# Optimization experiments

Measured on AMD Instinct MI355X. Metric: run time of the kernel, lower is better.

The kernel has to match this reference:

```python
import jax, jax.numpy as jnp
import numpy as np

B, H, W, D = 4, 64, 64, 384
M, P = 12, 9
DH = D // M             # 32 head dim
DFF = 3 * D             # 1152 FFN hidden
N = H * W               # 4096 queries (single level)


def setup_inputs():
    key = jax.random.key(0)
    ks = jax.random.split(key, 12)
    g = lambda k, s, sc=0.02: jax.random.normal(k, s, jnp.float32) * sc
    return {
        "x": jax.random.normal(ks[0], (B, D, H, W), jnp.float32),
        "qry_masks": jnp.zeros((B, H, W), jnp.float32),
        "so_w": g(ks[1], (M * P * 2, D)), "so_b": g(ks[2], (M * P * 2,)),
        "aw_w": g(ks[3], (M * P, D)), "aw_b": g(ks[4], (M * P,)),
        "vp_w": g(ks[5], (D, D)), "vp_b": jnp.zeros((D,), jnp.float32),
        "op_w": g(ks[6], (D, D)), "op_b": jnp.zeros((D,), jnp.float32),
        "ln1_g": jnp.ones((D,), jnp.float32), "ln1_b": jnp.zeros((D,), jnp.float32),
        "w1": g(ks[7], (DFF, D)), "w2": g(ks[8], (D, DFF)),
        "ln2_g": jnp.ones((D,), jnp.float32), "ln2_b": jnp.zeros((D,), jnp.float32),
        "level_embed": g(ks[9], (1, D), 1.0),
    }


def _layernorm(x, g, b, eps=1e-5):
    mu = x.mean(-1, keepdims=True)
    v = ((x - mu) ** 2).mean(-1, keepdims=True)
    return (x - mu) * jax.lax.rsqrt(v + eps) * g + b


def _sine_pos(mask):
    # mask: [B,H,W] bool. mmdet SinePositionalEncoding(num_feats=D//2, normalize=True)
    not_mask = (~mask).astype(jnp.float32)
    y = jnp.cumsum(not_mask, 1)
    x = jnp.cumsum(not_mask, 2)
    eps, scale = 1e-6, 2.0 * np.pi
    y = y / (y[:, -1:, :] + eps) * scale
    x = x / (x[:, :, -1:] + eps) * scale
    nf = D // 2
    dim_t = 10000.0 ** (2.0 * (jnp.arange(nf) // 2).astype(jnp.float32) / nf)
    px, py = x[..., None] / dim_t, y[..., None] / dim_t

    def interleave(p):
        return jnp.stack([jnp.sin(p[..., 0::2]), jnp.cos(p[..., 1::2])], -1).reshape(p.shape[:-1] + (nf,))

    return jnp.concatenate([interleave(py), interleave(px)], -1)  # [B,H,W,D]


def _bilinear_gather(v, px, py):
    # v: [B,M,HW,DH]; px,py: [B,M,NP] pixel coords (grid_sample align_corners=False, zero pad)
    x0 = jnp.floor(px); y0 = jnp.floor(py)
    lx, ly = px - x0, py - y0
    x0i, y0i = x0.astype(jnp.int32), y0.astype(jnp.int32)
    out = jnp.zeros(v.shape[:2] + (px.shape[-1], v.shape[-1]), v.dtype)
    for dx, dy, wgt in ((0, 0, (1 - lx) * (1 - ly)), (1, 0, lx * (1 - ly)),
                        (0, 1, (1 - lx) * ly), (1, 1, lx * ly)):
        xi, yi = x0i + dx, y0i + dy
        valid = ((xi >= 0) & (xi < W) & (yi >= 0) & (yi < H)).astype(v.dtype)
        idx = jnp.clip(yi, 0, H - 1) * W + jnp.clip(xi, 0, W - 1)
        g = jnp.take_along_axis(v, idx[..., None], axis=2)  # [B,M,NP,DH]
        out = out + (wgt * valid)[..., None] * g
    return out


def _msdeform_attn(q, value_in, ref, mask_flat,
                   so_w, so_b, aw_w, aw_b, vp_w, vp_b, op_w, op_b):
    value = value_in @ vp_w.T + vp_b                      # [B,N,D]
    value = jnp.where(mask_flat[..., None], 0.0, value)
    so = (q @ so_w.T + so_b).reshape(B, N, M, P, 2)       # single level
    aw = jax.nn.softmax((q @ aw_w.T + aw_b).reshape(B, N, M, P), axis=-1)
    norm = jnp.array([W, H], jnp.float32)
    loc = ref[:, :, None, None, :] + so / norm            # [B,N,M,P,2] in [0,1]
    v = value.reshape(B, N, M, DH).transpose(0, 2, 1, 3)  # [B,M,HW,DH]
    px = (loc[..., 0] * W - 0.5).transpose(0, 2, 1, 3).reshape(B, M, N * P)
    py = (loc[..., 1] * H - 0.5).transpose(0, 2, 1, 3).reshape(B, M, N * P)
    sampled = _bilinear_gather(v, px, py).reshape(B, M, N, P, DH)
    out = jnp.einsum('bmnpd,bnmp->bnmd', sampled, aw).reshape(B, N, D)
    return out @ op_w.T + op_b


def reference(x, qry_masks, so_w, so_b, aw_w, aw_b, vp_w, vp_b, op_w, op_b,
              ln1_g, ln1_b, w1, w2, ln2_g, ln2_b, level_embed):
    mask = (qry_masks == 255.0)                           # [B,H,W] bool
    pos = _sine_pos(mask).reshape(B, N, D) + level_embed[0]
    src = x.reshape(B, D, N).transpose(0, 2, 1)           # [B,N,D]
    mask_flat = mask.reshape(B, N)
    gy, gx = jnp.meshgrid((jnp.arange(H, dtype=jnp.float32) + 0.5) / H,
                          (jnp.arange(W, dtype=jnp.float32) + 0.5) / W, indexing='ij')
    ref = jnp.stack([gx.reshape(-1), gy.reshape(-1)], -1)[None]  # [1,N,2] (x,y)
    q = src
    attn = _msdeform_attn(q + pos, q, ref, mask_flat,
                          so_w, so_b, aw_w, aw_b, vp_w, vp_b, op_w, op_b)
    q = _layernorm(q + attn, ln1_g, ln1_b)
    q = _layernorm(q + jax.nn.relu(q @ w1.T) @ w2.T, ln2_g, ln2_b)
    return q.transpose(0, 2, 1).reshape(B, D, H, W)
```

## Files before the change

### kernel.cpp

```cpp
#include <hip/hip_runtime.h>
#include <math.h>

#define Bc   4
#define Hc   64
#define Wc   64
#define Dc   384
#define Nc   4096
#define Mc   12
#define Pc   9
#define DHc  32
#define DFFc 1152
#define BNc  (Bc*Nc)

typedef __attribute__((ext_vector_type(8))) short short8;
typedef __attribute__((ext_vector_type(4))) short short4v;
typedef __attribute__((ext_vector_type(4))) float floatx4;

__device__ __forceinline__ ushort f2bf(float f) {
    union { float f; unsigned u; } v; v.f = f;
    unsigned r = v.u + 0x7fffu + ((v.u >> 16) & 1u);
    return (ushort)(r >> 16);
}
__device__ __forceinline__ float bf2f(ushort u) {
    union { unsigned u; float f; } v; v.u = (unsigned)u << 16; return v.f;
}

__device__ __forceinline__ void gload_lds16(const void* g, void* l) {
    __builtin_amdgcn_global_load_lds(
        (const __attribute__((address_space(1))) void*)(uintptr_t)g,
        (__attribute__((address_space(3))) void*)(uintptr_t)l,
        16, 0, 0);
}


#define SOW_N  82944
#define AWW_N  41472
#define VPW_N  147456
#define OPW_N  147456
#define W1_N   442368
#define W2_N   442368
#define WTOT   1304064

__global__ void init_kernel(const float* __restrict__ so_w,
                            const float* __restrict__ aw_w,
                            const float* __restrict__ vp_w,
                            const float* __restrict__ op_w,
                            const float* __restrict__ w1,
                            const float* __restrict__ w2,
                            const float* __restrict__ so_b,
                            const float* __restrict__ aw_b,
                            ushort* __restrict__ out,
                            float* __restrict__ bias_out) {
    int i = blockIdx.x * 256 + threadIdx.x;
    if (i < WTOT) {
        float v;
        int j = i;
        if (j < SOW_N) v = so_w[j];
        else if ((j -= SOW_N) < AWW_N) v = aw_w[j];
        else if ((j -= AWW_N) < VPW_N) v = vp_w[j];
        else if ((j -= VPW_N) < OPW_N) v = op_w[j];
        else if ((j -= OPW_N) < W1_N)  v = w1[j];
        else { j -= W1_N; v = w2[j]; }
        out[i] = f2bf(v);
        return;
    }
    int j = i - WTOT;
    if (j < 384) {
        bias_out[j] = (j < 216) ? so_b[j] : (j < 324 ? aw_b[j - 216] : 0.f);
    }
}

__global__ __launch_bounds__(256) void cumsum_kernel(
        const float* __restrict__ qmask,
        float* __restrict__ cum_y, float* __restrict__ cum_x) {
    __shared__ float nm[64 * 65];
    __shared__ float ot[64 * 65];
    int b = blockIdx.x;
    int t = threadIdx.x;
    const float* qm = qmask + b * 4096;
    #pragma unroll
    for (int k = 0; k < 16; ++k) {
        int idx = t + k * 256;
        nm[(idx >> 6) * 65 + (idx & 63)] = (qm[idx] == 255.0f) ? 0.f : 1.f;
    }
    __syncthreads();
    if (t < 64) {
        float run = 0.f;
        for (int h = 0; h < 64; ++h) { run += nm[h * 65 + t]; ot[h * 65 + t] = run; }
    }
    __syncthreads();
    #pragma unroll
    for (int k = 0; k < 16; ++k) {
        int idx = t + k * 256;
        cum_y[b * 4096 + idx] = ot[(idx >> 6) * 65 + (idx & 63)];
    }
    __syncthreads();
    if (t < 64) {
        float run = 0.f;
        for (int w = 0; w < 64; ++w) { run += nm[t * 65 + w]; ot[t * 65 + w] = run; }
    }
    __syncthreads();
    #pragma unroll
    for (int k = 0; k < 16; ++k) {
        int idx = t + k * 256;
        cum_x[b * 4096 + idx] = ot[(idx >> 6) * 65 + (idx & 63)];
    }
}

__global__ void transpose_pos_kernel(const float* __restrict__ x,
                                     const float* __restrict__ cum_y,
                                     const float* __restrict__ cum_x,
                                     const float* __restrict__ level_embed,
                                     ushort* __restrict__ src_bf,
                                     ushort* __restrict__ qpos_bf) {
    __shared__ float tile[32][33];
    int b  = blockIdx.z;
    int n0 = blockIdx.x * 32, d0 = blockIdx.y * 32;
    int tx = threadIdx.x, ty = threadIdx.y;
    tile[ty][tx] = x[((size_t)b * Dc + (d0 + ty)) * Nc + (n0 + tx)];
    __syncthreads();
    int n = n0 + ty, d = d0 + tx;
    float v = tile[tx][ty];
    size_t oi = ((size_t)b * Nc + n) * Dc + d;
    src_bf[oi] = f2bf(v);
    int h = n >> 6, w = n & 63;
    const float TWO_PI = 6.28318530717958647692f;
    float vy = cum_y[(b * Hc + h) * Wc + w] /
               (cum_y[(b * Hc + (Hc - 1)) * Wc + w] + 1e-6f) * TWO_PI;
    float vx = cum_x[(b * Hc + h) * Wc + w] /
               (cum_x[(b * Hc + h) * Wc + (Wc - 1)] + 1e-6f) * TWO_PI;
    int   i  = (d < 192) ? d : d - 192;
    float vv = (d < 192) ? vy : vx;
    float e   = (float)(i >> 1) * (2.0f / 192.0f);
    float idt = exp2f(e * -13.28771237954945f);
    float ang = vv * idt;
    float pe  = (i & 1) ? __cosf(ang) : __sinf(ang);
    qpos_bf[oi] = f2bf(v + pe + level_embed[d]);
}

template <int KT>
__device__ __forceinline__ void gemm_core(
        const ushort* __restrict__ A, const ushort* __restrict__ Wt,
        const float* __restrict__ bias,
        float* __restrict__ Cf, ushort* __restrict__ Cb,
        int Nout, int relu, const float* __restrict__ qmask,
        ushort* As, ushort* Bs) {
    constexpr int NCH = KT / 32;
    const int tid  = threadIdx.x;
    const int m0   = blockIdx.x * 128;
    const int n0   = blockIdx.y * 128;
    const int lane = tid & 63;
    const int wv   = tid >> 6;
    const int wr   = (wv >> 1) * 64;
    const int wc   = (wv & 1) * 64;
    const int quad = lane >> 4;
    const int lrow = lane & 15;
    const int srow = wv * 32 + (lane >> 2);
    const int ssw  = (((lane & 3) ^ ((lane >> 2) & 3))) * 8;
    const int rsw  = (quad ^ (lrow & 3)) * 8;

    floatx4 acc[4][4];
    #pragma unroll
    for (int i = 0; i < 4; ++i)
        #pragma unroll
        for (int j = 0; j < 4; ++j)
            acc[i][j] = (floatx4)(0.f);

    #pragma unroll
    for (int s = 0; s < 2; ++s) {
        gload_lds16(A  + (size_t)(m0 + srow + s * 16) * KT + ssw,
                    As + wv * 1024 + s * 512);
        gload_lds16(Wt + (size_t)(n0 + srow + s * 16) * KT + ssw,
                    Bs + wv * 1024 + s * 512);
    }

    for (int c = 0; c < NCH; ++c) {
        const int cur = c & 1;
        __syncthreads();
        if (c + 1 < NCH) {
            const int k0 = (c + 1) * 32;
            #pragma unroll
            for (int s = 0; s < 2; ++s) {
                gload_lds16(A  + (size_t)(m0 + srow + s * 16) * KT + k0 + ssw,
                            As + (cur ^ 1) * 4096 + wv * 1024 + s * 512);
                gload_lds16(Wt + (size_t)(n0 + srow + s * 16) * KT + k0 + ssw,
                            Bs + (cur ^ 1) * 4096 + wv * 1024 + s * 512);
            }
        }
        short8 afr[4], bfr[4];
        #pragma unroll
        for (int i = 0; i < 4; ++i)
            afr[i] = *(const short8*)(As + cur * 4096 +
                                      (wr + i * 16 + lrow) * 32 + rsw);
        #pragma unroll
        for (int j = 0; j < 4; ++j)
            bfr[j] = *(const short8*)(Bs + cur * 4096 +
                                      (wc + j * 16 + lrow) * 32 + rsw);
        #pragma unroll
        for (int i = 0; i < 4; ++i)
            #pragma unroll
            for (int j = 0; j < 4; ++j)
                acc[i][j] = __builtin_amdgcn_mfma_f32_16x16x32_bf16(
                    afr[i], bfr[j], acc[i][j], 0, 0, 0);
    }

    float mz[4][4];
    #pragma unroll
    for (int i = 0; i < 4; ++i)
        #pragma unroll
        for (int r = 0; r < 4; ++r) {
            int row = m0 + wr + i * 16 + quad * 4 + r;
            mz[i][r] = (qmask && qmask[row] == 255.0f) ? 0.f : 1.f;
        }

    #pragma unroll
    for (int i = 0; i < 4; ++i) {
        #pragma unroll
        for (int j = 0; j < 4; ++j) {
            int col = n0 + wc + j * 16 + lrow;
            if (col >= Nout) continue;
            float bsv = bias ? bias[col] : 0.f;
            #pragma unroll
            for (int r = 0; r < 4; ++r) {
                int row = m0 + wr + i * 16 + quad * 4 + r;
                float v = acc[i][j][r] + bsv;
                if (relu) v = fmaxf(v, 0.f);
                v *= mz[i][r];
                if (Cf) Cf[(size_t)row * Nout + col] = v;
                if (Cb) Cb[(size_t)row * Nout + col] = f2bf(v);
            }
        }
    }
}

__global__ __launch_bounds__(256) void gemm_dual_kernel(
        const ushort* __restrict__ A0, const ushort* __restrict__ W0,
        const float* __restrict__ b0, float* __restrict__ Cf0,
        const ushort* __restrict__ A1, const ushort* __restrict__ W1,
        const float* __restrict__ b1, ushort* __restrict__ Cb1,
        const float* __restrict__ qmask) {
    __shared__ ushort As[2 * 128 * 32];
    __shared__ ushort Bs[2 * 128 * 32];
    if (blockIdx.z == 0)
        gemm_core<384>(A0, W0, b0, Cf0, nullptr, 384, 0, nullptr, As, Bs);
    else
        gemm_core<384>(A1, W1, b1, nullptr, Cb1, 384, 0, qmask, As, Bs);
}

template <int KT>
__global__ __launch_bounds__(512) void gemm_fullrow_kernel(
        const ushort* __restrict__ A, const ushort* __restrict__ Wt,
        const float* __restrict__ bias, const void* __restrict__ resid,
        const float* __restrict__ g, const float* __restrict__ beta,
        float* __restrict__ outf, ushort* __restrict__ outb) {
    constexpr int NCH = KT / 32;
    __shared__ ushort As[4 * 2048];
    __shared__ ushort Bs[4 * 12288];
    __shared__ float eps1[8][64], eps2[8][64];
    __shared__ float mu_l[64], rs_l[64];
    const int tid  = threadIdx.x;
    const int lane = tid & 63;
    const int wv   = tid >> 6;
    const int quad = lane >> 4;
    const int lrow = lane & 15;
    const int m0   = blockIdx.x * 64;
    const int srow = lane >> 2;
    const int ssw  = (((lane & 3) ^ ((lane >> 2) & 3))) * 8;
    const int rsw  = (quad ^ (lrow & 3)) * 8;

    floatx4 acc[4][3];
    #pragma unroll
    for (int i = 0; i < 4; ++i)
        #pragma unroll
        for (int j = 0; j < 3; ++j)
            acc[i][j] = (floatx4)(0.f);

#define STAGE_CHUNK(c, buf)                                                   \
    {   const int k0_ = (c) * 32;                                             \
        if (wv < 4)                                                           \
            gload_lds16(A + (size_t)(m0 + wv * 16 + srow) * KT + k0_ + ssw,   \
                        As + (buf) * 2048 + wv * 512);                        \
        _Pragma("unroll")                                                     \
        for (int s_ = 0; s_ < 3; ++s_)                                        \
            gload_lds16(Wt + (size_t)(wv * 48 + s_ * 16 + srow) * KT + k0_ + ssw, \
                        Bs + (buf) * 12288 + wv * 1536 + s_ * 512);           \
    }

    STAGE_CHUNK(0, 0)
    STAGE_CHUNK(1, 1)
    STAGE_CHUNK(2, 2)

    #pragma unroll
    for (int c = 0; c < NCH; ++c) {
        const int rem = (NCH - 1 - c) >= 2 ? 2 : (NCH - 1 - c);
        if (wv < 4) {
            if (rem == 2)      asm volatile("s_waitcnt vmcnt(8)" ::: "memory");
            else if (rem == 1) asm volatile("s_waitcnt vmcnt(4)" ::: "memory");
            else               asm volatile("s_waitcnt vmcnt(0)" ::: "memory");
        } else {
            if (rem == 2)      asm volatile("s_waitcnt vmcnt(6)" ::: "memory");
            else if (rem == 1) asm volatile("s_waitcnt vmcnt(3)" ::: "memory");
            else               asm volatile("s_waitcnt vmcnt(0)" ::: "memory");
        }
        __builtin_amdgcn_s_barrier();
        __builtin_amdgcn_sched_barrier(0);
        if (c + 3 < NCH) { STAGE_CHUNK(c + 3, (c + 3) & 3) }
        const int buf = c & 3;
        short8 afr[4], bfr[3];
        #pragma unroll
        for (int i = 0; i < 4; ++i)
            afr[i] = *(const short8*)(As + buf * 2048 +
                                      (i * 16 + lrow) * 32 + rsw);
        #pragma unroll
        for (int j = 0; j < 3; ++j)
            bfr[j] = *(const short8*)(Bs + buf * 12288 +
                                      (wv * 48 + j * 16 + lrow) * 32 + rsw);
        #pragma unroll
        for (int i = 0; i < 4; ++i)
            #pragma unroll
            for (int j = 0; j < 3; ++j)
                acc[i][j] = __builtin_amdgcn_mfma_f32_16x16x32_bf16(
                    afr[i], bfr[j], acc[i][j], 0, 0, 0);
    }
#undef STAGE_CHUNK

    float s1[16], s2[16];
    #pragma unroll
    for (int k = 0; k < 16; ++k) { s1[k] = 0.f; s2[k] = 0.f; }
    #pragma unroll
    for (int i = 0; i < 4; ++i) {
        #pragma unroll
        for (int r = 0; r < 4; ++r) {
            int rl = i * 16 + quad * 4 + r;
            #pragma unroll
            for (int j = 0; j < 3; ++j) {
                int col = wv * 48 + j * 16 + lrow;
                float t = acc[i][j][r];
                if (bias) t += bias[col];
                t += bf2f(((const ushort*)resid)[(size_t)(m0 + rl) * Dc + col]);
                acc[i][j][r] = t;
                s1[i * 4 + r] += t;
                s2[i * 4 + r] += t * t;
            }
        }
    }
    #pragma unroll
    for (int mm = 1; mm < 16; mm <<= 1) {
        #pragma unroll
        for (int k = 0; k < 16; ++k) {
            s1[k] += __shfl_xor(s1[k], mm);
            s2[k] += __shfl_xor(s2[k], mm);
        }
    }
    if (lrow == 0) {
        #pragma unroll
        for (int i = 0; i < 4; ++i)
            #pragma unroll
            for (int r = 0; r < 4; ++r) {
                int rl = i * 16 + quad * 4 + r;
                eps1[wv][rl] = s1[i * 4 + r];
                eps2[wv][rl] = s2[i * 4 + r];
            }
    }
    __syncthreads();
    if (tid < 64) {
        float a1 = 0.f, a2 = 0.f;
        #pragma unroll
        for (int w = 0; w < 8; ++w) { a1 += eps1[w][tid]; a2 += eps2[w][tid]; }
        float mu  = a1 * (1.0f / Dc);
        float var = a2 * (1.0f / Dc) - mu * mu;
        mu_l[tid] = mu;
        rs_l[tid] = rsqrtf(var + 1e-5f);
    }
    __syncthreads();
    #pragma unroll
    for (int i = 0; i < 4; ++i) {
        #pragma unroll
        for (int r = 0; r < 4; ++r) {
            int rl = i * 16 + quad * 4 + r;
            float mu = mu_l[rl], rs = rs_l[rl];
            #pragma unroll
            for (int j = 0; j < 3; ++j) {
                int col = wv * 48 + j * 16 + lrow;
                float v = (acc[i][j][r] - mu) * rs * g[col] + beta[col];
                outf[(size_t)(m0 + rl) * Dc + col] = v;
                outb[(size_t)(m0 + rl) * Dc + col] = f2bf(v);
            }
        }
    }
}

__global__ __launch_bounds__(512) void ffn_fused_kernel(
        const ushort* __restrict__ A,
        const ushort* __restrict__ W1b,
        const ushort* __restrict__ W2b,
        const float* __restrict__ resid,
        const float* __restrict__ g, const float* __restrict__ beta,
        float* __restrict__ outf) {
    __shared__ ushort smem[73728];
    ushort* Ast = smem;
    ushort* Hs  = smem + 24576;
    ushort* W1s = smem + 32768;
    ushort* W2s = smem + 49152;
    __shared__ float eps1[8][64], eps2[8][64];
    __shared__ float mu_l[64], rs_l[64];

    const int tid  = threadIdx.x;
    const int lane = tid & 63;
    const int wv   = tid >> 6;
    const int quad = lane >> 4;
    const int lrow = lane & 15;
    const int m0   = blockIdx.x * 64;
    const int ssw  = (((lane & 3) ^ ((lane >> 2) & 3))) * 8;
    const int rsw  = (quad ^ (lrow & 3)) * 8;

    ushort* W1w = W1s + wv * 2048;
    ushort* W2w = W2s + wv * 3072;

    floatx4 acc2[4][3];
    #pragma unroll
    for (int i = 0; i < 4; ++i)
        #pragma unroll
        for (int j = 0; j < 3; ++j)
            acc2[i][j] = (floatx4)(0.f);

#define STAGE_W1(hcv, kcv, buf)                                               \
    gload_lds16(W1b + (size_t)((hcv) * 128 + wv * 16 + (lane >> 2)) * 384 + (kcv) * 32 + ssw, \
                W1w + (buf) * 512 + lane * 8);

#define STAGE_W2(hcv, kc2v, buf)                                              \
    _Pragma("unroll")                                                         \
    for (int s_ = 0; s_ < 3; ++s_)                                            \
        gload_lds16(W2b + (size_t)(wv * 48 + s_ * 16 + (lane >> 2)) * 1152 + (hcv) * 128 + (kc2v) * 32 + ssw, \
                    W2w + (buf) * 1536 + s_ * 512 + lane * 8);

    #pragma unroll
    for (int k = 0; k < 6; ++k) {
        int l   = tid + 512 * k;
        int kc_ = l >> 8;
        int rem = l & 255;
        int sc_ = ((rem & 3) ^ ((rem >> 2) & 3)) * 8;
        gload_lds16(A + (size_t)(m0 + (rem >> 2)) * 384 + kc_ * 32 + sc_,
                    Ast + l * 8);
    }
    STAGE_W1(0, 0, 0)
    STAGE_W1(0, 1, 1)
    STAGE_W1(0, 2, 2)
    asm volatile("s_waitcnt vmcnt(3)" ::: "memory");
    __builtin_amdgcn_sched_barrier(0);
    __builtin_amdgcn_s_barrier();
    __builtin_amdgcn_sched_barrier(0);

    floatx4 acc1[4];
    for (int hc = 0; hc < 9; ++hc) {
        #pragma unroll
        for (int i = 0; i < 4; ++i) acc1[i] = (floatx4)(0.f);

        #pragma unroll
        for (int kc = 0; kc < 12; ++kc) {
            if (kc <= 8)       { STAGE_W1(hc, kc + 3, (kc + 3) & 3) }
            else if (kc == 9)  { STAGE_W2(hc, 0, 0) }
            else if (kc == 10) { STAGE_W2(hc, 1, 1) }
            if (kc <= 8)       asm volatile("s_waitcnt vmcnt(3)" ::: "memory");
            else if (kc == 9)  asm volatile("s_waitcnt vmcnt(5)" ::: "memory");
            else if (kc == 10) asm volatile("s_waitcnt vmcnt(7)" ::: "memory");
            else               asm volatile("s_waitcnt vmcnt(6)" ::: "memory");
            short8 afr[4], bfr;
            #pragma unroll
            for (int i = 0; i < 4; ++i)
                afr[i] = *(const short8*)(Ast + kc * 2048 +
                                          (i * 16 + lrow) * 32 + rsw);
            bfr = *(const short8*)(W1w + (kc & 3) * 512 + lrow * 32 + rsw);
            #pragma unroll
            for (int i = 0; i < 4; ++i)
                acc1[i] = __builtin_amdgcn_mfma_f32_16x16x32_bf16(
                    bfr, afr[i], acc1[i], 0, 0, 0);
        }

        #pragma unroll
        for (int i = 0; i < 4; ++i) {
            short4v pk;
            #pragma unroll
            for (int r = 0; r < 4; ++r)
                pk[r] = (short)f2bf(fmaxf(acc1[i][r], 0.f));
            int mrow = i * 16 + lrow;
            int slot = ((wv & 1) * 4 + quad) ^ (mrow & 6);
            *(short4v*)(Hs + (wv >> 1) * 2048 + mrow * 32 + slot * 4) = pk;
        }
        asm volatile("s_waitcnt lgkmcnt(0)" ::: "memory");
        __builtin_amdgcn_sched_barrier(0);
        __builtin_amdgcn_s_barrier();
        __builtin_amdgcn_sched_barrier(0);

        #pragma unroll
        for (int kc2 = 0; kc2 < 4; ++kc2) {
            if (kc2 == 0)      asm volatile("s_waitcnt vmcnt(3)" ::: "memory");
            else if (kc2 == 1) asm volatile("s_waitcnt vmcnt(4)" ::: "memory");
            else if (kc2 == 2) asm volatile("s_waitcnt vmcnt(5)" ::: "memory");
            else               asm volatile("s_waitcnt vmcnt(2)" ::: "memory");
            short8 afr[4], bfr[3];
            #pragma unroll
            for (int i = 0; i < 4; ++i) {
                int mrow = i * 16 + lrow;
                int s0 = (quad * 2) ^ (mrow & 6);
                afr[i] = *(const short8*)(Hs + kc2 * 2048 + mrow * 32 + s0 * 4);
            }
            #pragma unroll
            for (int j = 0; j < 3; ++j)
                bfr[j] = *(const short8*)(W2w + (kc2 & 1) * 1536 +
                                          (j * 16 + lrow) * 32 + rsw);
            asm volatile("s_waitcnt lgkmcnt(0)" ::: "memory");
            __builtin_amdgcn_sched_barrier(0);
            if (kc2 == 0)      { STAGE_W2(hc, 2, 0) STAGE_W1(hc + 1, 0, 0) }
            else if (kc2 == 1) { STAGE_W2(hc, 3, 1) STAGE_W1(hc + 1, 1, 1) }
            else if (kc2 == 2) { STAGE_W1(hc + 1, 2, 2) }
            #pragma unroll
            for (int i = 0; i < 4; ++i)
                #pragma unroll
                for (int j = 0; j < 3; ++j)
                    acc2[i][j] = __builtin_amdgcn_mfma_f32_16x16x32_bf16(
                        afr[i], bfr[j], acc2[i][j], 0, 0, 0);
        }
        asm volatile("s_waitcnt lgkmcnt(0)" ::: "memory");
        __builtin_amdgcn_sched_barrier(0);
        __builtin_amdgcn_s_barrier();
        __builtin_amdgcn_sched_barrier(0);
    }
    asm volatile("s_waitcnt vmcnt(0)" ::: "memory");
#undef STAGE_W1
#undef STAGE_W2

    float s1[16], s2[16];
    #pragma unroll
    for (int k = 0; k < 16; ++k) { s1[k] = 0.f; s2[k] = 0.f; }
    #pragma unroll
    for (int i = 0; i < 4; ++i) {
        #pragma unroll
        for (int r = 0; r < 4; ++r) {
            int rl = i * 16 + quad * 4 + r;
            #pragma unroll
            for (int j = 0; j < 3; ++j) {
                int col = wv * 48 + j * 16 + lrow;
                float t = acc2[i][j][r];
                t += resid[(size_t)(m0 + rl) * Dc + col];
                acc2[i][j][r] = t;
                s1[i * 4 + r] += t;
                s2[i * 4 + r] += t * t;
            }
        }
    }
    #pragma unroll
    for (int mm = 1; mm < 16; mm <<= 1) {
        #pragma unroll
        for (int k = 0; k < 16; ++k) {
            s1[k] += __shfl_xor(s1[k], mm);
            s2[k] += __shfl_xor(s2[k], mm);
        }
    }
    if (lrow == 0) {
        #pragma unroll
        for (int i = 0; i < 4; ++i)
            #pragma unroll
            for (int r = 0; r < 4; ++r) {
                int rl = i * 16 + quad * 4 + r;
                eps1[wv][rl] = s1[i * 4 + r];
                eps2[wv][rl] = s2[i * 4 + r];
            }
    }
    __syncthreads();
    if (tid < 64) {
        float a1 = 0.f, a2 = 0.f;
        #pragma unroll
        for (int w = 0; w < 8; ++w) { a1 += eps1[w][tid]; a2 += eps2[w][tid]; }
        float mu  = a1 * (1.0f / Dc);
        float var = a2 * (1.0f / Dc) - mu * mu;
        mu_l[tid] = mu;
        rs_l[tid] = rsqrtf(var + 1e-5f);
    }
    __syncthreads();
    #pragma unroll
    for (int i = 0; i < 4; ++i) {
        #pragma unroll
        for (int r = 0; r < 4; ++r) {
            int rl = i * 16 + quad * 4 + r;
            float mu = mu_l[rl], rs = rs_l[rl];
            #pragma unroll
            for (int j = 0; j < 3; ++j) {
                int col = wv * 48 + j * 16 + lrow;
                acc2[i][j][r] = (acc2[i][j][r] - mu) * rs * g[col] + beta[col];
            }
        }
    }
    float* tile = (float*)smem;
    const int b   = m0 >> 12;
    const int n0r = m0 & 4095;
    #pragma unroll
    for (int gp = 0; gp < 2; ++gp) {
        __syncthreads();
        if ((wv >> 2) == gp) {
            int cbase = (wv & 3) * 48;
            #pragma unroll
            for (int i = 0; i < 4; ++i)
                #pragma unroll
                for (int j = 0; j < 3; ++j) {
                    int c = cbase + j * 16 + lrow;
                    #pragma unroll
                    for (int r = 0; r < 4; ++r) {
                        int rl = i * 16 + quad * 4 + r;
                        tile[rl * 193 + c] = acc2[i][j][r];
                    }
                }
        }
        __syncthreads();
        const int row = tid & 63;
        const int cp  = tid >> 6;
        #pragma unroll
        for (int it = 0; it < 24; ++it) {
            int c = it * 8 + cp;
            outf[((size_t)(b * Dc + gp * 192 + c)) * Nc + n0r + row] =
                tile[row * 193 + c];
        }
    }
}

__global__ __launch_bounds__(256) void deform_attn_kernel(
        const ushort* __restrict__ value_bf, const float* __restrict__ soaw,
        ushort* __restrict__ out) {
    int bid   = blockIdx.x;
    int slice = bid % 48;
    int h     = bid / 48;
    int m  = slice % Mc;
    int b  = slice / Mc;
    int w  = threadIdx.x >> 2;
    int l4 = threadIdx.x & 3;
    int n  = (h << 6) | w;
    int bn = b * Nc + n;
    const float* sop = soaw + (size_t)bn * 384 + m * 18;
    const float* lgt = soaw + (size_t)bn * 384 + 216 + m * Pc;
    float awv[Pc];
    float mx = lgt[0];
    #pragma unroll
    for (int i = 1; i < Pc; ++i) mx = fmaxf(mx, lgt[i]);
    float ssum = 0.f;
    #pragma unroll
    for (int i = 0; i < Pc; ++i) { awv[i] = __expf(lgt[i] - mx); ssum += awv[i]; }
    float sinv = 1.f / ssum;
    const ushort* vb = value_bf + ((size_t)b * Nc) * Dc + m * DHc + l4 * 8;
    float acc[8] = {0.f, 0.f, 0.f, 0.f, 0.f, 0.f, 0.f, 0.f};
    #pragma unroll
    for (int p = 0; p < Pc; ++p) {
        float2 so2 = *(const float2*)(sop + p * 2);
        float px = (float)w + so2.x;
        float py = (float)h + so2.y;
        float x0f = floorf(px), y0f = floorf(py);
        float lx = px - x0f, ly = py - y0f;
        int x0 = (int)x0f, y0 = (int)y0f;
        int x1 = x0 + 1,  y1 = y0 + 1;
        float a = awv[p] * sinv;
        float w00 = (1.f - lx) * (1.f - ly) * a;
        float w01 = lx * (1.f - ly) * a;
        float w10 = (1.f - lx) * ly * a;
        float w11 = lx * ly * a;
        bool bx0 = (unsigned)x0 < 64u, bx1 = (unsigned)x1 < 64u;
        bool by0 = (unsigned)y0 < 64u, by1 = (unsigned)y1 < 64u;
        w00 = (bx0 && by0) ? w00 : 0.f;
        w01 = (bx1 && by0) ? w01 : 0.f;
        w10 = (bx0 && by1) ? w10 : 0.f;
        w11 = (bx1 && by1) ? w11 : 0.f;
        int cx0 = min(max(x0, 0), 63), cx1 = min(max(x1, 0), 63);
        int cy0 = min(max(y0, 0), 63), cy1 = min(max(y1, 0), 63);
        uint4 q00 = *(const uint4*)(vb + (size_t)(cy0 * 64 + cx0) * Dc);
        uint4 q01 = *(const uint4*)(vb + (size_t)(cy0 * 64 + cx1) * Dc);
        uint4 q10 = *(const uint4*)(vb + (size_t)(cy1 * 64 + cx0) * Dc);
        uint4 q11 = *(const uint4*)(vb + (size_t)(cy1 * 64 + cx1) * Dc);
        union { unsigned u; float f; } t;
        #define ACC2(word, wg, k)                                   \
            t.u = (word) << 16;         acc[k]     += (wg) * t.f;   \
            t.u = (word) & 0xffff0000u; acc[k + 1] += (wg) * t.f;
        #define ACC8(q, wg) \
            ACC2((q).x, wg, 0) ACC2((q).y, wg, 2) ACC2((q).z, wg, 4) ACC2((q).w, wg, 6)
        ACC8(q00, w00) ACC8(q01, w01) ACC8(q10, w10) ACC8(q11, w11)
        #undef ACC8
        #undef ACC2
    }
    short8 o;
    #pragma unroll
    for (int k = 0; k < 8; ++k) o[k] = (short)f2bf(acc[k]);
    *(short8*)(out + (size_t)bn * Dc + m * DHc + l4 * 8) = o;
}

extern "C" void kernel_launch(void* const* d_in, const int* in_sizes, int n_in,
                              void* d_out, int out_size, void* d_ws, size_t ws_size,
                              hipStream_t stream) {
    (void)in_sizes; (void)n_in; (void)out_size; (void)ws_size;
    const float* x      = (const float*)d_in[0];
    const float* qmask  = (const float*)d_in[1];
    const float* so_w   = (const float*)d_in[2];
    const float* so_b   = (const float*)d_in[3];
    const float* aw_w   = (const float*)d_in[4];
    const float* aw_b   = (const float*)d_in[5];
    const float* vp_w   = (const float*)d_in[6];
    const float* vp_b   = (const float*)d_in[7];
    const float* op_w   = (const float*)d_in[8];
    const float* op_b   = (const float*)d_in[9];
    const float* ln1_g  = (const float*)d_in[10];
    const float* ln1_b  = (const float*)d_in[11];
    const float* w1     = (const float*)d_in[12];
    const float* w2     = (const float*)d_in[13];
    const float* ln2_g  = (const float*)d_in[14];
    const float* ln2_b  = (const float*)d_in[15];
    const float* lvl    = (const float*)d_in[16];
    float* out = (float*)d_out;

    float*  ws       = (float*)d_ws;
    float*  q1_f     = ws;
    ushort* src_bf   = (ushort*)(q1_f + 6291456);
    ushort* qpos_bf  = src_bf + 6291456;
    ushort* value_bf = qpos_bf + 6291456;
    ushort* hbuf_bf  = value_bf + 6291456;
    float*  soaw_f   = (float*)hbuf_bf;
    ushort* wbuf     = hbuf_bf + 18874368;
    float*  soaw_bias= (float*)(wbuf + 1304064);
    float*  cum_y    = soaw_bias + 384;
    float*  cum_x    = cum_y + 16384;

    const ushort* soaw_wb = wbuf;
    const ushort* vp_wb = soaw_wb + SOW_N + AWW_N;
    const ushort* op_wb = vp_wb + VPW_N;
    const ushort* w1_b  = op_wb + OPW_N;
    const ushort* w2_b  = w1_b + W1_N;

    init_kernel<<<(WTOT + 384 + 255) / 256, 256, 0, stream>>>(
        so_w, aw_w, vp_w, op_w, w1, w2, so_b, aw_b, wbuf, soaw_bias);
    cumsum_kernel<<<Bc, 256, 0, stream>>>(qmask, cum_y, cum_x);
    transpose_pos_kernel<<<dim3(Nc / 32, Dc / 32, Bc), dim3(32, 32), 0, stream>>>(
        x, cum_y, cum_x, lvl, src_bf, qpos_bf);
    gemm_dual_kernel<<<dim3(BNc / 128, 3, 2), 256, 0, stream>>>(
        qpos_bf, soaw_wb, soaw_bias, soaw_f,
        src_bf, vp_wb, vp_b, value_bf, qmask);
    deform_attn_kernel<<<3072, 256, 0, stream>>>(
        value_bf, soaw_f, qpos_bf);
    gemm_fullrow_kernel<384><<<BNc / 64, 512, 0, stream>>>(
        qpos_bf, op_wb, op_b, src_bf, ln1_g, ln1_b, q1_f, qpos_bf);
    ffn_fused_kernel<<<BNc / 64, 512, 0, stream>>>(
        qpos_bf, w1_b, w2_b, q1_f, ln2_g, ln2_b, out);
}
```

Measured before the change: 256.3 us.

## Load FFN weight fragments directly into registers instead of staging through LDS

The fused FFN kernel stops staging W1/W2 tiles through LDS via async global-to-LDS loads with hand-tuned vmcnt waits. Each wave now loads its W1 and W2 MFMA operand fragments straight from global memory into registers and prefetches the next hidden chunk's fragments after the current use. This cuts LDS usage from about 147KB to 64KB, which may allow higher occupancy, and removes the LDS reads for B operands. In exchange it adds many vector registers per thread and relies on compiler-inserted waits, so global load latency may be less well hidden.

```diff
diff --git a/kernel.cpp b/kernel.cpp
--- a/kernel.cpp
+++ b/kernel.cpp
@@ -31,7 +31,6 @@
         (__attribute__((address_space(3))) void*)(uintptr_t)l,
         16, 0, 0);
 }
-
 
 #define SOW_N  82944
 #define AWW_N  41472
@@ -397,11 +396,9 @@
         const float* __restrict__ resid,
         const float* __restrict__ g, const float* __restrict__ beta,
         float* __restrict__ outf) {
-    __shared__ ushort smem[73728];
+    __shared__ ushort smem[32768];
     ushort* Ast = smem;
     ushort* Hs  = smem + 24576;
-    ushort* W1s = smem + 32768;
-    ushort* W2s = smem + 49152;
     __shared__ float eps1[8][64], eps2[8][64];
     __shared__ float mu_l[64], rs_l[64];
 
@@ -411,11 +408,10 @@
     const int quad = lane >> 4;
     const int lrow = lane & 15;
     const int m0   = blockIdx.x * 64;
-    const int ssw  = (((lane & 3) ^ ((lane >> 2) & 3))) * 8;
     const int rsw  = (quad ^ (lrow & 3)) * 8;
 
-    ushort* W1w = W1s + wv * 2048;
-    ushort* W2w = W2s + wv * 3072;
+    const ushort* w1base = W1b + (size_t)(wv * 16 + lrow) * 384 + quad * 8;
+    const ushort* w2base = W2b + (size_t)(wv * 48 + lrow) * 1152 + quad * 8;
 
     floatx4 acc2[4][3];
     #pragma unroll
@@ -423,16 +419,6 @@
         #pragma unroll
         for (int j = 0; j < 3; ++j)
             acc2[i][j] = (floatx4)(0.f);
-
-#define STAGE_W1(hcv, kcv, buf)                                               \
-    gload_lds16(W1b + (size_t)((hcv) * 128 + wv * 16 + (lane >> 2)) * 384 + (kcv) * 32 + ssw, \
-                W1w + (buf) * 512 + lane * 8);
-
-#define STAGE_W2(hcv, kc2v, buf)                                              \
-    _Pragma("unroll")                                                         \
-    for (int s_ = 0; s_ < 3; ++s_)                                            \
-        gload_lds16(W2b + (size_t)(wv * 48 + s_ * 16 + (lane >> 2)) * 1152 + (hcv) * 128 + (kc2v) * 32 + ssw, \
-                    W2w + (buf) * 1536 + s_ * 512 + lane * 8);
 
     #pragma unroll
     for (int k = 0; k < 6; ++k) {
@@ -443,10 +429,18 @@
         gload_lds16(A + (size_t)(m0 + (rem >> 2)) * 384 + kc_ * 32 + sc_,
                     Ast + l * 8);
     }
-    STAGE_W1(0, 0, 0)
-    STAGE_W1(0, 1, 1)
-    STAGE_W1(0, 2, 2)
-    asm volatile("s_waitcnt vmcnt(3)" ::: "memory");
+    __builtin_amdgcn_sched_barrier(0);
+    short8 w1f[12], w2f[4][3];
+    #pragma unroll
+    for (int k = 0; k < 12; ++k)
+        w1f[k] = *(const short8*)(w1base + (size_t)k * 32);
+    #pragma unroll
+    for (int k2 = 0; k2 < 4; ++k2)
+        #pragma unroll
+        for (int j = 0; j < 3; ++j)
+            w2f[k2][j] = *(const short8*)(w2base + (size_t)j * 18432 + k2 * 32);
+    __builtin_amdgcn_sched_barrier(0);
+    asm volatile("s_waitcnt vmcnt(24)" ::: "memory");
     __builtin_amdgcn_sched_barrier(0);
     __builtin_amdgcn_s_barrier();
     __builtin_amdgcn_sched_barrier(0);
@@ -458,23 +452,21 @@
 
         #pragma unroll
         for (int kc = 0; kc < 12; ++kc) {
-            if (kc <= 8)       { STAGE_W1(hc, kc + 3, (kc + 3) & 3) }
-            else if (kc == 9)  { STAGE_W2(hc, 0, 0) }
-            else if (kc == 10) { STAGE_W2(hc, 1, 1) }
-            if (kc <= 8)       asm volatile("s_waitcnt vmcnt(3)" ::: "memory");
-            else if (kc == 9)  asm volatile("s_waitcnt vmcnt(5)" ::: "memory");
-            else if (kc == 10) asm volatile("s_waitcnt vmcnt(7)" ::: "memory");
-            else               asm volatile("s_waitcnt vmcnt(6)" ::: "memory");
-            short8 afr[4], bfr;
+            short8 afr[4];
             #pragma unroll
             for (int i = 0; i < 4; ++i)
                 afr[i] = *(const short8*)(Ast + kc * 2048 +
                                           (i * 16 + lrow) * 32 + rsw);
-            bfr = *(const short8*)(W1w + (kc & 3) * 512 + lrow * 32 + rsw);
             #pragma unroll
             for (int i = 0; i < 4; ++i)
                 acc1[i] = __builtin_amdgcn_mfma_f32_16x16x32_bf16(
-                    bfr, afr[i], acc1[i], 0, 0, 0);
+                    w1f[kc], afr[i], acc1[i], 0, 0, 0);
+        }
+        if (hc + 1 < 9) {
+            #pragma unroll
+            for (int k = 0; k < 12; ++k)
+                w1f[k] = *(const short8*)(w1base + (size_t)(hc + 1) * 49152 +
+                                          (size_t)k * 32);
         }
 
         #pragma unroll
@@ -494,11 +486,7 @@
 
         #pragma unroll
         for (int kc2 = 0; kc2 < 4; ++kc2) {
-            if (kc2 == 0)      asm volatile("s_waitcnt vmcnt(3)" ::: "memory");
-            else if (kc2 == 1) asm volatile("s_waitcnt vmcnt(4)" ::: "memory");
-            else if (kc2 == 2) asm volatile("s_waitcnt vmcnt(5)" ::: "memory");
-            else               asm volatile("s_waitcnt vmcnt(2)" ::: "memory");
-            short8 afr[4], bfr[3];
+            short8 afr[4];
             #pragma unroll
             for (int i = 0; i < 4; ++i) {
                 int mrow = i * 16 + lrow;
@@ -506,29 +494,25 @@
                 afr[i] = *(const short8*)(Hs + kc2 * 2048 + mrow * 32 + s0 * 4);
             }
             #pragma unroll
-            for (int j = 0; j < 3; ++j)
-                bfr[j] = *(const short8*)(W2w + (kc2 & 1) * 1536 +
-                                          (j * 16 + lrow) * 32 + rsw);
-            asm volatile("s_waitcnt lgkmcnt(0)" ::: "memory");
-            __builtin_amdgcn_sched_barrier(0);
-            if (kc2 == 0)      { STAGE_W2(hc, 2, 0) STAGE_W1(hc + 1, 0, 0) }
-            else if (kc2 == 1) { STAGE_W2(hc, 3, 1) STAGE_W1(hc + 1, 1, 1) }
-            else if (kc2 == 2) { STAGE_W1(hc + 1, 2, 2) }
-            #pragma unroll
             for (int i = 0; i < 4; ++i)
                 #pragma unroll
                 for (int j = 0; j < 3; ++j)
                     acc2[i][j] = __builtin_amdgcn_mfma_f32_16x16x32_bf16(
-                        afr[i], bfr[j], acc2[i][j], 0, 0, 0);
+                        afr[i], w2f[kc2][j], acc2[i][j], 0, 0, 0);
+        }
+        if (hc + 1 < 9) {
+            #pragma unroll
+            for (int k2 = 0; k2 < 4; ++k2)
+                #pragma unroll
+                for (int j = 0; j < 3; ++j)
+                    w2f[k2][j] = *(const short8*)(w2base + (size_t)j * 18432 +
+                                                  (hc + 1) * 128 + k2 * 32);
         }
         asm volatile("s_waitcnt lgkmcnt(0)" ::: "memory");
         __builtin_amdgcn_sched_barrier(0);
         __builtin_amdgcn_s_barrier();
         __builtin_amdgcn_sched_barrier(0);
     }
-    asm volatile("s_waitcnt vmcnt(0)" ::: "memory");
-#undef STAGE_W1
-#undef STAGE_W2
 
     float s1[16], s2[16];
     #pragma unroll
```

Measured after the change: 267.9 us. +4.5%, slower.
